# Kernel tuning notes

Hardware: AMD Instinct MI355X
Metric: run time of the kernel (lower is better)

## Reference

```python
import jax, jax.numpy as jnp
import numpy as np
from math import factorial

MUL = 64
LS = (0, 1, 2)            # node irrep l's, each with multiplicity MUL
SH_LS = (0, 1, 2)         # edge spherical-harmonics l's (lmax=2)
NODE_DIM = MUL * sum(2 * l + 1 for l in LS)  # 576
# uvu instructions (i_node, j_sh, k_out) from the original selection rule ir_k in ir_i*ir_j
INSTRUCTIONS = [(0, 0, 0), (0, 1, 1), (0, 2, 2), (1, 0, 1), (1, 1, 0), (1, 1, 2),
                (1, 2, 1), (2, 0, 2), (2, 1, 1), (2, 2, 0), (2, 2, 2)]
N_PATHS = {0: 3, 1: 4, 2: 4}          # number of instructions writing each output irrep
N_TP_W = len(INSTRUCTIONS) * MUL      # 704 per-edge TP weights
N_NODES, N_EDGES = 10000, 100000


def _su2_cg(j1, j2, j3, m1, m2, m3):
    # Clebsch-Gordan <j1 m1 j2 m2 | j3 m3> via Racah formula (integer j)
    if m1 + m2 != m3:
        return 0.0
    f = factorial
    pref = ((2 * j3 + 1)
            * f(j1 + j2 - j3) * f(j1 - j2 + j3) * f(-j1 + j2 + j3) / f(j1 + j2 + j3 + 1)
            * f(j1 + m1) * f(j1 - m1) * f(j2 + m2) * f(j2 - m2) * f(j3 + m3) * f(j3 - m3)) ** 0.5
    s = 0.0
    for k in range(0, j1 + j2 + j3 + 1):
        d = [k, j1 + j2 - j3 - k, j1 - m1 - k, j2 + m2 - k, j3 - j2 + m1 + k, j3 - j1 - m2 + k]
        if any(t < 0 for t in d):
            continue
        s += (-1) ** k / np.prod([float(f(t)) for t in d])
    return pref * s


def _q(l):
    # real -> complex spherical harmonic change of basis (e3nn convention, phase makes CG real)
    q = np.zeros((2 * l + 1, 2 * l + 1), dtype=complex)
    for m in range(-l, 0):
        q[l + m, l + abs(m)] = 1 / 2 ** 0.5
        q[l + m, l - abs(m)] = -1j / 2 ** 0.5
    q[l, l] = 1.0
    for m in range(1, l + 1):
        q[l + m, l + abs(m)] = (-1) ** m / 2 ** 0.5
        q[l + m, l - abs(m)] = 1j * (-1) ** m / 2 ** 0.5
    return (-1j) ** l * q


def _real_cg(l1, l2, l3):
    cg = np.zeros((2 * l1 + 1, 2 * l2 + 1, 2 * l3 + 1), dtype=complex)
    for a, m1 in enumerate(range(-l1, l1 + 1)):
        for b, m2 in enumerate(range(-l2, l2 + 1)):
            for c, m3 in enumerate(range(-l3, l3 + 1)):
                cg[a, b, c] = _su2_cg(l1, l2, l3, m1, m2, m3)
    C = np.einsum('ij,kl,nm,ikn->jlm', _q(l1), _q(l2), np.conj(_q(l3)), cg)
    C = C.real if np.abs(C.real).sum() >= np.abs(C.imag).sum() else C.imag
    return jnp.asarray(C / np.linalg.norm(C), dtype=jnp.float32)  # Frobenius-normalized (3j-style)


W3J = {}
for (_i, _j, _k) in INSTRUCTIONS:
    _key = (LS[_i], SH_LS[_j], LS[_k])
    if _key not in W3J:
        W3J[_key] = _real_cg(*_key)


def _sh(u):
    # component-normalized real spherical harmonics up to l=2 on unit vectors u: [E,3] -> [E,9]
    x, y, z = u[:, 0], u[:, 1], u[:, 2]
    s3 = 3.0 ** 0.5
    sh0 = jnp.ones_like(x)[:, None]
    sh1 = s3 * jnp.stack([y, z, x], -1)
    sh2 = 5.0 ** 0.5 * jnp.stack([s3 * x * y, s3 * y * z, 1.5 * z * z - 0.5,
                                  s3 * x * z, 0.5 * s3 * (x * x - y * y)], -1)
    return jnp.concatenate([sh0, sh1, sh2], -1)


def _blocks(t):
    # split [N, 576] into per-l blocks [N, MUL, 2l+1]
    out, off = [], 0
    for l in LS:
        d = 2 * l + 1
        out.append(t[:, off:off + MUL * d].reshape(-1, MUL, d))
        off += MUL * d
    return out


def _forward(node_feat, edge_vec, fc_w0, fc_w1, fc_w2, lin_w, src, dst):
    E, N = edge_vec.shape[0], node_feat.shape[0]
    dist = jnp.linalg.norm(edge_vec, axis=-1, keepdims=True)      # [E,1]
    sh = _sh(edge_vec / jnp.maximum(dist, 1e-9))                  # [E,9]
    # radial MLP (FullyConnectedNet-style: x @ W / sqrt(fan_in), silu on hidden layers)
    h = jax.nn.silu(dist @ fc_w0)
    h = jax.nn.silu(h @ fc_w1 / jnp.sqrt(64.0))
    tp_w = h @ fc_w2 / jnp.sqrt(64.0)                             # [E, 704]
    xb = _blocks(node_feat[src])                                  # gather source node feats
    sh_b, off = [], 0
    for l in SH_LS:
        d = 2 * l + 1
        sh_b.append(sh[:, off:off + d])
        off += d
    msg_b = [jnp.zeros((E, MUL, 2 * l + 1), node_feat.dtype) for l in LS]
    for n, (i, j, k) in enumerate(INSTRUCTIONS):                  # uvu channelwise tensor product
        C = W3J[(LS[i], SH_LS[j], LS[k])]
        w = tp_w[:, n * MUL:(n + 1) * MUL]                        # [E, MUL] per-edge path weights
        alpha = ((2 * LS[k] + 1.0) / N_PATHS[k]) ** 0.5           # component/path normalization
        msg_b[k] = msg_b[k] + alpha * jnp.einsum('abc,eua,eb,eu->euc', C, xb[i], sh_b[j], w)
    msg = jnp.concatenate([m.reshape(E, -1) for m in msg_b], -1)  # [E,576]
    aggr = jax.ops.segment_sum(msg, dst, num_segments=N)          # scatter-add over destination
    ab = _blocks(aggr)
    out = jnp.concatenate(
        [(jnp.einsum('nud,uv->nvd', ab[l], lin_w[l]) / MUL ** 0.5).reshape(N, -1)
         for l in range(len(LS))], -1)                            # equivariant Linear per irrep
    return out + node_feat                                        # residual


def setup_inputs() -> dict:
    key = jax.random.key(0)
    ks = jax.random.split(key, 8)
    return {
        'node_feat': jax.random.normal(ks[0], (N_NODES, NODE_DIM), jnp.float32),
        'edge_index': jax.random.randint(ks[1], (2, N_EDGES), 0, N_NODES),
        'edge_vec': jax.random.normal(ks[2], (N_EDGES, 3), jnp.float32),
        'fc_w0': jax.random.normal(ks[3], (1, 64), jnp.float32),
        'fc_w1': jax.random.normal(ks[4], (64, 64), jnp.float32),
        'fc_w2': jax.random.normal(ks[5], (64, N_TP_W), jnp.float32),
        'lin_w': jax.random.normal(ks[6], (len(LS), MUL, MUL), jnp.float32),
    }


def reference(node_feat, edge_index, edge_vec, fc_w0, fc_w1, fc_w2, lin_w):
    src, dst = edge_index[0], edge_index[1]
    return _forward(node_feat, edge_vec, fc_w0, fc_w1, fc_w2, lin_w, src, dst)
```

## Files before the change

kernel.cpp:

```cpp
#include <hip/hip_runtime.h>
#include <hip/hip_fp16.h>
#include <cmath>
#include <complex>

#define MULT 64
#define NODE_DIM 576
#define TE 8
#define PB 64

typedef _Float16 half8_t __attribute__((ext_vector_type(8)));
typedef _Float16 half4_t __attribute__((ext_vector_type(4)));
typedef float    floatx4 __attribute__((ext_vector_type(4)));

typedef std::complex<double> cd;

static double factd(int n){ double r=1; for(int i=2;i<=n;i++) r*=(double)i; return r; }

static double su2_cg(int j1,int j2,int j3,int m1,int m2,int m3){
  if(m1+m2!=m3) return 0.0;
  double pref = (2*j3+1)*factd(j1+j2-j3)*factd(j1-j2+j3)*factd(-j1+j2+j3)/factd(j1+j2+j3+1)
              * factd(j1+m1)*factd(j1-m1)*factd(j2+m2)*factd(j2-m2)*factd(j3+m3)*factd(j3-m3);
  pref = std::sqrt(pref);
  double s=0;
  for(int k=0;k<=j1+j2+j3;k++){
    int d0=k, d1=j1+j2-j3-k, d2=j1-m1-k, d3=j2+m2-k, d4=j3-j2+m1+k, d5=j3-j1-m2+k;
    if(d0<0||d1<0||d2<0||d3<0||d4<0||d5<0) continue;
    double denom = factd(d0)*factd(d1)*factd(d2)*factd(d3)*factd(d4)*factd(d5);
    s += ((k&1)?-1.0:1.0)/denom;
  }
  return pref*s;
}

static void make_q(int l, cd q[5][5]){
  for(int i=0;i<5;i++)for(int j=0;j<5;j++) q[i][j]=cd(0,0);
  double s = 1.0/std::sqrt(2.0);
  for(int m=-l;m<0;m++){
    q[l+m][l-m] = cd(s,0);
    q[l+m][l+m] = cd(0,-s);
  }
  q[l][l]=cd(1,0);
  for(int m=1;m<=l;m++){
    double sg = (m&1)?-1.0:1.0;
    q[l+m][l+m]=cd(sg*s,0);
    q[l+m][l-m]=cd(0,sg*s);
  }
  cd ph = (l==0)?cd(1,0) : ((l==1)?cd(0,-1) : cd(-1,0));
  for(int i=0;i<2*l+1;i++)for(int j=0;j<2*l+1;j++) q[i][j]*=ph;
}

static void real_cg(int l1,int l2,int l3, double* out){
  int d1=2*l1+1,d2=2*l2+1,d3=2*l3+1;
  double cg[125];
  for(int a=0;a<d1;a++)for(int b=0;b<d2;b++)for(int c=0;c<d3;c++)
    cg[(a*d2+b)*d3+c] = su2_cg(l1,l2,l3,a-l1,b-l2,c-l3);
  cd q1[5][5],q2[5][5],q3[5][5];
  make_q(l1,q1); make_q(l2,q2); make_q(l3,q3);
  cd C[125];
  for(int t=0;t<d1*d2*d3;t++) C[t]=cd(0,0);
  for(int i=0;i<d1;i++)for(int k=0;k<d2;k++)for(int n=0;n<d3;n++){
    double v = cg[(i*d2+k)*d3+n];
    if(v==0.0) continue;
    for(int j=0;j<d1;j++){
      cd a = q1[i][j]*v;
      if(a.real()==0.0 && a.imag()==0.0) continue;
      for(int l=0;l<d2;l++){
        cd b = a*q2[k][l];
        for(int m=0;m<d3;m++) C[(j*d2+l)*d3+m] += b*std::conj(q3[n][m]);
      }
    }
  }
  double sre=0,sim=0;
  for(int t=0;t<d1*d2*d3;t++){ sre+=std::fabs(C[t].real()); sim+=std::fabs(C[t].imag()); }
  bool use_re = (sre>=sim);
  double nrm=0;
  for(int t=0;t<d1*d2*d3;t++){ double x=use_re?C[t].real():C[t].imag(); nrm+=x*x; }
  nrm=std::sqrt(nrm);
  for(int t=0;t<d1*d2*d3;t++){ double x=use_re?C[t].real():C[t].imag(); out[t]=x/nrm; }
}

struct CGPack { float v[363]; };

__device__ __forceinline__ float silu_f(float x){ return x/(1.f+expf(-x)); }
__host__ __device__ constexpr int LOFF(int l){ return l==0?0:(l==1?1:4); }

template<int DI,int DJ,int DK>
__device__ __forceinline__ void tp_add(const float* __restrict__ C, const float* xi,
                                       const float* sh, float wn, float* mk){
  float tmp[DK];
#pragma unroll
  for(int c=0;c<DK;c++) tmp[c]=0.f;
#pragma unroll
  for(int a=0;a<DI;a++){
#pragma unroll
    for(int b=0;b<DJ;b++){
      float p = xi[a]*sh[b];
#pragma unroll
      for(int c=0;c<DK;c++) tmp[c] = fmaf(C[(a*DJ+b)*DK+c], p, tmp[c]);
    }
  }
#pragma unroll
  for(int c=0;c<DK;c++) mk[c] = fmaf(wn, tmp[c], mk[c]);
}

__global__ void hist_kernel(const int* __restrict__ dst, int* __restrict__ cnt, int E){
  int i = blockIdx.x*blockDim.x + threadIdx.x;
  if(i<E) atomicAdd(&cnt[dst[i]], 1);
}

__global__ __launch_bounds__(1024) void scan_kernel(const int* __restrict__ cnt,
                                                    int* __restrict__ row_ptr, int N){
  __shared__ int s_part[1024];
  const int t = threadIdx.x;
  const int per = (N + 1023) >> 10;
  const int b0 = t*per, b1 = min(N, b0+per);
  int local = 0;
  for(int i=b0;i<b1;i++) local += cnt[i];
  s_part[t] = local;
  __syncthreads();
  for(int off=1; off<1024; off<<=1){
    int v = (t>=off) ? s_part[t-off] : 0;
    __syncthreads();
    s_part[t] += v;
    __syncthreads();
  }
  int run = (t==0) ? 0 : s_part[t-1];
  for(int i=b0;i<b1;i++){ row_ptr[i] = run; run += cnt[i]; }
  if(t==1023) row_ptr[N] = s_part[1023];
}

__global__ void fill_kernel(const int* __restrict__ dst, const int* __restrict__ row_ptr,
                            int* __restrict__ cnt2, int* __restrict__ sorted, int E){
  int i = blockIdx.x*blockDim.x + threadIdx.x;
  if(i<E){
    int d = dst[i];
    int pos = atomicAdd(&cnt2[d], 1);
    sorted[row_ptr[d]+pos] = i;
  }
}

__global__ void sortb_kernel(int* __restrict__ sorted, const int* __restrict__ row_ptr, int N){
  int n = blockIdx.x*blockDim.x + threadIdx.x;
  if(n>=N) return;
  int b=row_ptr[n], e=row_ptr[n+1];
  for(int i=b+1;i<e;i++){
    int v=sorted[i]; int j=i-1;
    while(j>=b && sorted[j]>v){ sorted[j+1]=sorted[j]; j--; }
    sorted[j+1]=v;
  }
}

__global__ void w2t_kernel(const float* __restrict__ w2, __half* __restrict__ w2t){
  int i = blockIdx.x*256 + threadIdx.x;
  if(i < 704*64){
    int col = i >> 6, k = i & 63;
    w2t[i] = (__half)w2[k*704 + col];
  }
}

template<typename TW>
__global__ __launch_bounds__(256,2) void emp_pre4_kernel(
  const float* __restrict__ evec, const float* __restrict__ w0,
  const float* __restrict__ w1, const __half* __restrict__ w2t,
  TW* __restrict__ tpw, float* __restrict__ shs, int E)
{
  __shared__ float     s_h0T[64][64];
  __shared__ float     s_tile[64][64];
  __shared__ _Float16  s_h1h[64][64];
  __shared__ _Float16  s_w2t[64][64];
  __shared__ float     s_d[PB];

  const int t   = threadIdx.x;
  const int eg  = t >> 4;
  const int ug  = t & 15;
  const int es0 = eg*4, u0 = ug*4;
  const int e0  = blockIdx.x*PB;

  if(t < PB){
    const int e = e0 + t;
    float dist = 0.f;
    if(e < E){
      float ex=evec[e*3+0], ey=evec[e*3+1], ez=evec[e*3+2];
      dist = sqrtf(ex*ex+ey*ey+ez*ez);
      float inv = 1.f/fmaxf(dist,1e-9f);
      float x=ex*inv, y=ey*inv, z=ez*inv;
      const float s3=1.7320508075688772f, s5=2.2360679774997896f;
      float* srow = shs + (size_t)e*12;
      srow[0]=1.f;
      srow[1]=s3*y; srow[2]=s3*z; srow[3]=s3*x;
      srow[4]=s5*s3*x*y; srow[5]=s5*s3*y*z; srow[6]=s5*(1.5f*z*z-0.5f);
      srow[7]=s5*s3*x*z; srow[8]=s5*0.5f*s3*(x*x-y*y);
    }
    s_d[t] = dist;
  }
#pragma unroll
  for(int r=0;r<16;r++){ int idx=t+r*256; s_tile[idx>>6][idx&63] = w1[idx]; }
  __syncthreads();

#pragma unroll
  for(int r=0;r<16;r++){
    int idx = t + r*256;
    int u = idx>>6, es = idx&63;
    s_h0T[u][es] = silu_f(s_d[es]*w0[u]);
  }
  __syncthreads();

  {
    float acc[4][4];
#pragma unroll
    for(int i=0;i<4;i++)
#pragma unroll
      for(int j=0;j<4;j++) acc[i][j]=0.f;
#pragma unroll 4
    for(int k=0;k<64;k++){
      float4 a = *(const float4*)&s_h0T[k][es0];
      float4 b = *(const float4*)&s_tile[k][u0];
      float av[4]={a.x,a.y,a.z,a.w};
      float bv[4]={b.x,b.y,b.z,b.w};
#pragma unroll
      for(int i=0;i<4;i++)
#pragma unroll
        for(int j=0;j<4;j++) acc[i][j]=fmaf(av[i],bv[j],acc[i][j]);
    }
#pragma unroll
    for(int i=0;i<4;i++){
      const int row = es0+i;
      const int ks  = u0 ^ ((row&7)<<3);
      half4_t hv;
#pragma unroll
      for(int j=0;j<4;j++) hv[j] = (_Float16)silu_f(acc[i][j]*0.125f);
      *(half4_t*)&s_h1h[row][ks] = hv;
    }
  }
  __syncthreads();

  const int lane = t & 63;
  const int w    = t >> 6;
  const int lr   = lane & 15;
  const int lk   = lane >> 4;
  half8_t fA0, fA1;
  {
    const int row = w*16 + lr;
    const int swz = (row&7)<<3;
    fA0 = *(half8_t*)&s_h1h[row][(     lk*8) ^ swz];
    fA1 = *(half8_t*)&s_h1h[row][(32 + lk*8) ^ swz];
  }

  for(int n=0;n<11;n++){
    __syncthreads();
#pragma unroll
    for(int r=0;r<2;r++){
      int c8  = t + r*256;
      int col = c8 >> 3;
      int k8  = (c8 & 7) << 3;
      int ks  = k8 ^ ((col & 7) << 3);
      *(uint4*)&s_w2t[col][ks] =
        *(const uint4*)&w2t[(size_t)(n*64+col)*64 + k8];
    }
    __syncthreads();
#pragma unroll
    for(int cg=0; cg<4; cg++){
      const int colB = cg*16 + lr;
      const int swzB = (colB&7)<<3;
      half8_t fB0 = *(half8_t*)&s_w2t[colB][(     lk*8) ^ swzB];
      half8_t fB1 = *(half8_t*)&s_w2t[colB][(32 + lk*8) ^ swzB];
      floatx4 acc = {0.f,0.f,0.f,0.f};
      acc = __builtin_amdgcn_mfma_f32_16x16x32_f16(fA0, fB0, acc, 0,0,0);
      acc = __builtin_amdgcn_mfma_f32_16x16x32_f16(fA1, fB1, acc, 0,0,0);
#pragma unroll
      for(int r=0;r<4;r++){
        const int e = e0 + w*16 + lk*4 + r;
        if(e < E) tpw[(size_t)e*704 + n*64 + cg*16 + lr] = (TW)(acc[r]*0.125f);
      }
    }
  }
}

template<typename TW>
__global__ __launch_bounds__(256,1) void emp_gather4_kernel(
  const float* __restrict__ nf, const TW* __restrict__ tpw,
  const float* __restrict__ shs, const int* __restrict__ sorted,
  const int* __restrict__ row_ptr, const int* __restrict__ src_idx,
  const float* __restrict__ lw, float* __restrict__ out, int NN, CGPack cgp)
{
  __shared__ float s_a[4][NODE_DIM];
  const int t = threadIdx.x;
  const int u = t & 63;
  const int w = t >> 6;
  const int n = blockIdx.x*4 + w;
  const bool vn = (n < NN);

  float H0[1]={0.f}, H1[3]={0.f}, H2[5]={0.f}, H3[3]={0.f}, H4[9]={0.f},
        H5[9]={0.f}, H6[15]={0.f}, H7[5]={0.f}, H8[15]={0.f},
        H9[25]={0.f}, H10[25]={0.f};

#define ACC(N_, XA, DI, DJ, JO, WN, SH)                                      \
      {                                                                      \
        const float wnl = WN[N_];                                            \
        _Pragma("unroll")                                                    \
        for(int b=0;b<(DJ);b++){                                             \
          float z = wnl*SH[(JO)+b];                                          \
          _Pragma("unroll")                                                  \
          for(int a=0;a<(DI);a++)                                            \
            H##N_[a*(DJ)+b] = fmaf(XA[a], z, H##N_[a*(DJ)+b]);               \
        }                                                                    \
      }
#define ACC_ALL(X0, X1, X2, WN, SH)                                          \
      ACC(0, X0,1,1,0,WN,SH) ACC(1, X0,1,3,1,WN,SH) ACC(2, X0,1,5,4,WN,SH)   \
      ACC(3, X1,3,1,0,WN,SH) ACC(4, X1,3,3,1,WN,SH) ACC(5, X1,3,3,1,WN,SH)   \
      ACC(6, X1,3,5,4,WN,SH) ACC(7, X2,5,1,0,WN,SH) ACC(8, X2,5,3,1,WN,SH)   \
      ACC(9, X2,5,5,4,WN,SH) ACC(10,X2,5,5,4,WN,SH)

  if(vn){
    const int beg = row_ptr[n], end = row_ptr[n+1];
    int i = beg;
    for(; i+1<end; i+=2){
      const int eA = __builtin_amdgcn_readfirstlane(sorted[i]);
      const int eB = __builtin_amdgcn_readfirstlane(sorted[i+1]);
      const int sA = __builtin_amdgcn_readfirstlane(src_idx[eA]);
      const int sB = __builtin_amdgcn_readfirstlane(src_idx[eB]);
      const float* xrA = nf + (size_t)sA*NODE_DIM;
      const float* xrB = nf + (size_t)sB*NODE_DIM;
      const TW*    wrA = tpw + (size_t)eA*704;
      const TW*    wrB = tpw + (size_t)eB*704;
      const float* srA = shs + (size_t)eA*12;
      const float* srB = shs + (size_t)eB*12;
      float x0A[1]={xrA[u]}, x0B[1]={xrB[u]};
      float x1A[3], x1B[3], x2A[5], x2B[5], shA[9], shB[9], wnA[11], wnB[11];
#pragma unroll
      for(int a=0;a<3;a++){ x1A[a]=xrA[64+u*3+a]; x1B[a]=xrB[64+u*3+a]; }
#pragma unroll
      for(int a=0;a<5;a++){ x2A[a]=xrA[256+u*5+a]; x2B[a]=xrB[256+u*5+a]; }
#pragma unroll
      for(int j=0;j<9;j++){ shA[j]=srA[j]; shB[j]=srB[j]; }
#pragma unroll
      for(int m=0;m<11;m++){ wnA[m]=(float)wrA[m*64+u]; wnB[m]=(float)wrB[m*64+u]; }
      ACC_ALL(x0A,x1A,x2A,wnA,shA)
      ACC_ALL(x0B,x1B,x2B,wnB,shB)
    }
    if(i<end){
      const int eA = __builtin_amdgcn_readfirstlane(sorted[i]);
      const int sA = __builtin_amdgcn_readfirstlane(src_idx[eA]);
      const float* xrA = nf + (size_t)sA*NODE_DIM;
      const TW*    wrA = tpw + (size_t)eA*704;
      const float* srA = shs + (size_t)eA*12;
      float x0A[1]={xrA[u]};
      float x1A[3], x2A[5], shA[9], wnA[11];
#pragma unroll
      for(int a=0;a<3;a++) x1A[a]=xrA[64+u*3+a];
#pragma unroll
      for(int a=0;a<5;a++) x2A[a]=xrA[256+u*5+a];
#pragma unroll
      for(int j=0;j<9;j++) shA[j]=srA[j];
#pragma unroll
      for(int m=0;m<11;m++) wnA[m]=(float)wrA[m*64+u];
      ACC_ALL(x0A,x1A,x2A,wnA,shA)
    }
  }
#undef ACC_ALL
#undef ACC

  float mg[9];
#pragma unroll
  for(int i=0;i<9;i++) mg[i]=0.f;
#define CGA(N_, DI, DJ, DK, OFF, KO)                                         \
  _Pragma("unroll")                                                          \
  for(int a=0;a<(DI);a++)                                                    \
    _Pragma("unroll")                                                        \
    for(int b=0;b<(DJ);b++){                                                 \
      float h = H##N_[a*(DJ)+b];                                             \
      _Pragma("unroll")                                                      \
      for(int c=0;c<(DK);c++)                                                \
        mg[(KO)+c] = fmaf(cgp.v[(OFF)+(a*(DJ)+b)*(DK)+c], h, mg[(KO)+c]);    \
    }
  CGA(0, 1,1,1, 0,   0)
  CGA(1, 1,3,3, 1,   1)
  CGA(2, 1,5,5, 10,  4)
  CGA(3, 3,1,3, 35,  1)
  CGA(4, 3,3,1, 44,  0)
  CGA(5, 3,3,5, 53,  4)
  CGA(6, 3,5,3, 98,  1)
  CGA(7, 5,1,5, 143, 4)
  CGA(8, 5,3,3, 168, 1)
  CGA(9, 5,5,1, 213, 0)
  CGA(10,5,5,5, 238, 4)
#undef CGA

  s_a[w][u] = mg[0];
#pragma unroll
  for(int d=0;d<3;d++) s_a[w][(1+d)*64+u] = mg[1+d];
#pragma unroll
  for(int d=0;d<5;d++) s_a[w][(4+d)*64+u] = mg[4+d];
  __syncthreads();

  if(vn){
    const int v = u;
    float o0=0.f, o1[3]={0.f,0.f,0.f}, o2[5]={0.f,0.f,0.f,0.f,0.f};
#pragma unroll 8
    for(int uu=0;uu<64;uu++){
      float wv0 = lw[uu*64+v];
      o0 = fmaf(s_a[w][uu], wv0, o0);
      float wv1 = lw[4096+uu*64+v];
#pragma unroll
      for(int d=0;d<3;d++) o1[d]=fmaf(s_a[w][(1+d)*64+uu],wv1,o1[d]);
      float wv2 = lw[8192+uu*64+v];
#pragma unroll
      for(int d=0;d<5;d++) o2[d]=fmaf(s_a[w][(4+d)*64+uu],wv2,o2[d]);
    }
    const float* nrow = nf + (size_t)n*NODE_DIM;
    float* orow = out + (size_t)n*NODE_DIM;
    orow[v] = fmaf(o0,0.125f,nrow[v]);
#pragma unroll
    for(int d=0;d<3;d++) orow[64+v*3+d]=fmaf(o1[d],0.125f,nrow[64+v*3+d]);
#pragma unroll
    for(int d=0;d<5;d++) orow[256+v*5+d]=fmaf(o2[d],0.125f,nrow[256+v*5+d]);
  }
}

__global__ __launch_bounds__(64) void emp_node_kernel(
  const float* __restrict__ nf, const float* __restrict__ lw,
  float* __restrict__ out, int N)
{
  __shared__ float s_a[NODE_DIM];
  const int n = blockIdx.x;
  const int v = threadIdx.x;
  float* orow = out + (size_t)n*NODE_DIM;
#pragma unroll
  for(int r=0;r<9;r++) s_a[r*64+v] = orow[r*64+v];
  __syncthreads();

  float o0=0.f, o1[3]={0.f,0.f,0.f}, o2[5]={0.f,0.f,0.f,0.f,0.f};
#pragma unroll 8
  for(int uu=0;uu<64;uu++){
    float wv0 = lw[uu*64+v];
    o0 = fmaf(s_a[uu], wv0, o0);
    float wv1 = lw[4096+uu*64+v];
#pragma unroll
    for(int d=0;d<3;d++) o1[d]=fmaf(s_a[64+uu*3+d],wv1,o1[d]);
    float wv2 = lw[8192+uu*64+v];
#pragma unroll
    for(int d=0;d<5;d++) o2[d]=fmaf(s_a[256+uu*5+d],wv2,o2[d]);
  }
  const float* nrow = nf + (size_t)n*NODE_DIM;
  orow[v] = fmaf(o0,0.125f,nrow[v]);
#pragma unroll
  for(int d=0;d<3;d++) orow[64+v*3+d]=fmaf(o1[d],0.125f,nrow[64+v*3+d]);
#pragma unroll
  for(int d=0;d<5;d++) orow[256+v*5+d]=fmaf(o2[d],0.125f,nrow[256+v*5+d]);
}

__global__ __launch_bounds__(512,1) void emp_pre_kernel(
  const float* __restrict__ evec, const float* __restrict__ w0,
  const float* __restrict__ w1, float* __restrict__ h1s,
  float* __restrict__ shs, int E)
{
  __shared__ float s_h0[TE][64];
  __shared__ float s_sh[TE][9];
  const int t=threadIdx.x, u=t&63, es=t>>6;
  const int e = blockIdx.x*TE+es;
  const bool valid = (e<E);
  float dist=0.f;
  if(valid){
    float ex=evec[e*3+0], ey=evec[e*3+1], ez=evec[e*3+2];
    dist = sqrtf(ex*ex+ey*ey+ez*ez);
    if(u==0){
      float inv = 1.f/fmaxf(dist,1e-9f);
      float x=ex*inv, y=ey*inv, z=ez*inv;
      const float s3=1.7320508075688772f, s5=2.2360679774997896f;
      s_sh[es][0]=1.f;
      s_sh[es][1]=s3*y; s_sh[es][2]=s3*z; s_sh[es][3]=s3*x;
      s_sh[es][4]=s5*s3*x*y; s_sh[es][5]=s5*s3*y*z; s_sh[es][6]=s5*(1.5f*z*z-0.5f);
      s_sh[es][7]=s5*s3*x*z; s_sh[es][8]=s5*0.5f*s3*(x*x-y*y);
    }
  }
  s_h0[es][u] = silu_f(dist * w0[u]);
  __syncthreads();
  if(valid && u<9) shs[(size_t)e*12+u] = s_sh[es][u];
  float acc = 0.f;
#pragma unroll
  for(int k=0;k<64;k++) acc = fmaf(s_h0[es][k], w1[k*64+u], acc);
  if(valid) h1s[(size_t)e*64+u] = silu_f(acc*0.125f);
}

__global__ __launch_bounds__(256,2) void emp_gather_kernel(
  const float* __restrict__ nf, const float* __restrict__ h1s,
  const float* __restrict__ shs, const int* __restrict__ sorted,
  const int* __restrict__ row_ptr, const int* __restrict__ src_idx,
  const float* __restrict__ w2, float* __restrict__ aggr, CGPack cgp)
{
  __shared__ float s_tile[64][64];
  __shared__ float s_x[8][576];
  __shared__ float s_h1[8][64];
  __shared__ float s_sh[8][12];
  __shared__ int   s_eid[8];
  __shared__ int   s_src[8];
  __shared__ float s_red[4][576];

  const int n = blockIdx.x;
  const int t = threadIdx.x;
  const int u = t & 63;
  const int w = t >> 6;
  const int beg = row_ptr[n], end = row_ptr[n+1];

  float mg[9];
#pragma unroll
  for(int i=0;i<9;i++) mg[i]=0.f;

  for(int base=beg; base<end; base+=8){
    const int C = min(8, end-base);
    if(t < C){ int e = sorted[base+t]; s_eid[t]=e; s_src[t]=src_idx[e]; }
    __syncthreads();
    for(int idx=t; idx<C*576; idx+=256){
      int c = idx/576, j = idx - 576*c;
      s_x[c][j] = nf[(size_t)s_src[c]*NODE_DIM + j];
    }
    for(int idx=t; idx<C*64; idx+=256){
      int c = idx>>6, j = idx&63;
      s_h1[c][j] = h1s[(size_t)s_eid[c]*64 + j];
    }
    if(t < C*12){
      int c = t/12, j = t - 12*c;
      if(j<9) s_sh[c][j] = shs[(size_t)s_eid[c]*12 + j];
    }
    __syncthreads();

#define GI(N_, LI, LJ, LK, OFF)                                              \
    {                                                                        \
      for(int idx=t; idx<4096; idx+=256){                                    \
        int k = idx>>6, j = idx&63;                                          \
        s_tile[k][j] = w2[k*704 + (N_)*64 + j];                              \
      }                                                                      \
      __syncthreads();                                                       \
      for(int c=w; c<C; c+=4){                                               \
        float wn = 0.f;                                                      \
        _Pragma("unroll")                                                    \
        for(int k=0;k<64;k++) wn = fmaf(s_h1[c][k], s_tile[k][u], wn);       \
        wn *= 0.125f;                                                        \
        const int xb = (LI)==0 ? u : ((LI)==1 ? 64+u*3 : 256+u*5);           \
        tp_add<2*(LI)+1,2*(LJ)+1,2*(LK)+1>(cgp.v+(OFF), &s_x[c][xb],         \
                                           &s_sh[c][LOFF(LJ)], wn,           \
                                           mg+LOFF(LK));                     \
      }                                                                      \
      __syncthreads();                                                       \
    }
    GI(0,0,0,0,0)
    GI(1,0,1,1,1)
    GI(2,0,2,2,10)
    GI(3,1,0,1,35)
    GI(4,1,1,0,44)
    GI(5,1,1,2,53)
    GI(6,1,2,1,98)
    GI(7,2,0,2,143)
    GI(8,2,1,1,168)
    GI(9,2,2,0,213)
    GI(10,2,2,2,238)
#undef GI
  }

  s_red[w][u] = mg[0];
#pragma unroll
  for(int a=0;a<3;a++) s_red[w][64+u*3+a] = mg[1+a];
#pragma unroll
  for(int a=0;a<5;a++) s_red[w][256+u*5+a] = mg[4+a];
  __syncthreads();
  float* arow = aggr + (size_t)n*NODE_DIM;
  for(int idx=t; idx<NODE_DIM; idx+=256)
    arow[idx] = s_red[0][idx]+s_red[1][idx]+s_red[2][idx]+s_red[3][idx];
}

extern "C" void kernel_launch(void* const* d_in, const int* in_sizes, int n_in,
                              void* d_out, int out_size, void* d_ws, size_t ws_size,
                              hipStream_t stream)
{
  const float* nf   = (const float*)d_in[0];
  const int*   eidx = (const int*)  d_in[1];
  const float* evec = (const float*)d_in[2];
  const float* w0   = (const float*)d_in[3];
  const float* w1   = (const float*)d_in[4];
  const float* w2   = (const float*)d_in[5];
  const float* lw   = (const float*)d_in[6];
  const int E = in_sizes[1]/2;
  const int N = in_sizes[0]/NODE_DIM;
  const int* src = eidx;
  const int* dst = eidx + E;

  CGPack cgp;
  {
    const int II[11]={0,0,0,1,1,1,1,2,2,2,2};
    const int JJ[11]={0,1,2,0,1,1,2,0,1,2,2};
    const int KK[11]={0,1,2,1,0,2,1,2,1,0,2};
    const int OFF[11]={0,1,10,35,44,53,98,143,168,213,238};
    const double npaths[3]={3.0,4.0,4.0};
    double tmp[125];
    for(int n=0;n<11;n++){
      int li=II[n], lj=JJ[n], lk=KK[n];
      real_cg(li,lj,lk,tmp);
      double alpha = std::sqrt((2.0*lk+1.0)/npaths[lk]);
      int sz=(2*li+1)*(2*lj+1)*(2*lk+1);
      for(int q=0;q<sz;q++) cgp.v[OFF[n]+q]=(float)(tmp[q]*alpha);
    }
  }

  auto align256 = [](size_t x){ return (x + 255) & ~(size_t)255; };

  auto layoutA = [&](size_t elemBytes, size_t& o_tpw, size_t& o_sh, size_t& o_w2t,
                     size_t& o_srt, size_t& o_cnt, size_t& o_rp)->size_t{
    size_t off = 0;
    o_tpw = off; off = align256(off + (size_t)E*704*elemBytes);
    o_sh  = off; off = align256(off + (size_t)E*12*sizeof(float));
    o_w2t = off; off = align256(off + (size_t)704*64*sizeof(__half));
    o_srt = off; off = align256(off + (size_t)E*sizeof(int));
    o_cnt = off; off = align256(off + (size_t)N*2*sizeof(int));
    o_rp  = off; off = align256(off + (size_t)(N+1)*sizeof(int));
    return off;
  };
  size_t a32_tpw,a32_sh,a32_w2t,a32_srt,a32_cnt,a32_rp;
  size_t a16_tpw,a16_sh,a16_w2t,a16_srt,a16_cnt,a16_rp;
  const size_t needA32 = layoutA(4, a32_tpw,a32_sh,a32_w2t,a32_srt,a32_cnt,a32_rp);
  const size_t needA16 = layoutA(2, a16_tpw,a16_sh,a16_w2t,a16_srt,a16_cnt,a16_rp);

  size_t offB = 0;
  size_t b_h1  = offB; offB = align256(offB + (size_t)E*64*sizeof(float));
  size_t b_sh  = offB; offB = align256(offB + (size_t)E*12*sizeof(float));
  size_t b_srt = offB; offB = align256(offB + (size_t)E*sizeof(int));
  size_t b_cnt = offB; offB = align256(offB + (size_t)N*2*sizeof(int));
  size_t b_rp  = offB; offB = align256(offB + (size_t)(N+1)*sizeof(int));

  char* ws = (char*)d_ws;

  auto runCSR = [&](int* cnt, int* cnt2, int* row_ptr, int* sorted){
    hipMemsetAsync(cnt, 0, (size_t)N*2*sizeof(int), stream);
    hipLaunchKernelGGL(hist_kernel, dim3((E+255)/256), dim3(256), 0, stream,
                       dst, cnt, E);
    hipLaunchKernelGGL(scan_kernel, dim3(1), dim3(1024), 0, stream,
                       cnt, row_ptr, N);
    hipLaunchKernelGGL(fill_kernel, dim3((E+255)/256), dim3(256), 0, stream,
                       dst, row_ptr, cnt2, sorted, E);
    hipLaunchKernelGGL(sortb_kernel, dim3((N+255)/256), dim3(256), 0, stream,
                       sorted, row_ptr, N);
  };

  const int nb3 = (N+3)/4;

  if(ws_size >= needA32){
    float*  tpw    = (float*) (ws + a32_tpw);
    float*  shs    = (float*) (ws + a32_sh);
    __half* w2t    = (__half*)(ws + a32_w2t);
    int*    sorted = (int*)   (ws + a32_srt);
    int*    cnt    = (int*)   (ws + a32_cnt);
    int*    cnt2   = cnt + N;
    int*    row_ptr= (int*)   (ws + a32_rp);
    hipLaunchKernelGGL(w2t_kernel, dim3((704*64+255)/256), dim3(256), 0, stream, w2, w2t);
    runCSR(cnt, cnt2, row_ptr, sorted);
    hipLaunchKernelGGL((emp_pre4_kernel<float>), dim3((E+PB-1)/PB), dim3(256), 0, stream,
                       evec, w0, w1, w2t, tpw, shs, E);
    hipLaunchKernelGGL((emp_gather4_kernel<float>), dim3(nb3), dim3(256), 0, stream,
                       nf, tpw, shs, sorted, row_ptr, src, lw, (float*)d_out, N, cgp);
  } else if(ws_size >= needA16){
    __half* tpw    = (__half*)(ws + a16_tpw);
    float*  shs    = (float*) (ws + a16_sh);
    __half* w2t    = (__half*)(ws + a16_w2t);
    int*    sorted = (int*)   (ws + a16_srt);
    int*    cnt    = (int*)   (ws + a16_cnt);
    int*    cnt2   = cnt + N;
    int*    row_ptr= (int*)   (ws + a16_rp);
    hipLaunchKernelGGL(w2t_kernel, dim3((704*64+255)/256), dim3(256), 0, stream, w2, w2t);
    runCSR(cnt, cnt2, row_ptr, sorted);
    hipLaunchKernelGGL((emp_pre4_kernel<__half>), dim3((E+PB-1)/PB), dim3(256), 0, stream,
                       evec, w0, w1, w2t, tpw, shs, E);
    hipLaunchKernelGGL((emp_gather4_kernel<__half>), dim3(nb3), dim3(256), 0, stream,
                       nf, tpw, shs, sorted, row_ptr, src, lw, (float*)d_out, N, cgp);
  } else {
    float* h1s    = (float*)(ws + b_h1);
    float* shs    = (float*)(ws + b_sh);
    int*   sorted = (int*)  (ws + b_srt);
    int*   cnt    = (int*)  (ws + b_cnt);
    int*   cnt2   = cnt + N;
    int*   row_ptr= (int*)  (ws + b_rp);
    runCSR(cnt, cnt2, row_ptr, sorted);
    hipLaunchKernelGGL(emp_pre_kernel, dim3((E+TE-1)/TE), dim3(512), 0, stream,
                       evec, w0, w1, h1s, shs, E);
    hipLaunchKernelGGL(emp_gather_kernel, dim3(N), dim3(256), 0, stream,
                       nf, h1s, shs, sorted, row_ptr, src, w2, (float*)d_out, cgp);
    hipLaunchKernelGGL(emp_node_kernel, dim3(N), dim3(64), 0, stream,
                       nf, lw, (float*)d_out, N);
  }
}
```

Baseline: 218.2 us.

## Store per-edge TP weights and SH in destination-sorted order, unroll gather by four

Adds a rank kernel that maps each edge to its position in the destination-sorted order and precomputes the sorted source indices. The pre kernel then writes per-edge TP weights and spherical harmonics at the sorted position, so the gather kernel reads them contiguously and skips the indirection through the sorted and src arrays. The gather loop is unrolled to four edges per iteration with vectorized SH loads to expose more memory-level parallelism. In exchange, the pre kernel's stores become scattered, an extra kernel launch is added, and register pressure rises in the gather.

```diff
diff --git a/kernel.cpp b/kernel.cpp
--- a/kernel.cpp
+++ b/kernel.cpp
@@ -149,6 +149,12 @@
   }
 }
 
+__global__ void rank_kernel(const int* __restrict__ sorted, const int* __restrict__ src_idx,
+                            int* __restrict__ rank, int* __restrict__ src_s, int E){
+  int i = blockIdx.x*blockDim.x + threadIdx.x;
+  if(i<E){ int e = sorted[i]; rank[e] = i; src_s[i] = src_idx[e]; }
+}
+
 __global__ void w2t_kernel(const float* __restrict__ w2, __half* __restrict__ w2t){
   int i = blockIdx.x*256 + threadIdx.x;
   if(i < 704*64){
@@ -161,6 +167,7 @@
 __global__ __launch_bounds__(256,2) void emp_pre4_kernel(
   const float* __restrict__ evec, const float* __restrict__ w0,
   const float* __restrict__ w1, const __half* __restrict__ w2t,
+  const int* __restrict__ rank,
   TW* __restrict__ tpw, float* __restrict__ shs, int E)
 {
   __shared__ float     s_h0T[64][64];
@@ -168,6 +175,7 @@
   __shared__ _Float16  s_h1h[64][64];
   __shared__ _Float16  s_w2t[64][64];
   __shared__ float     s_d[PB];
+  __shared__ int       s_rank[PB];
 
   const int t   = threadIdx.x;
   const int eg  = t >> 4;
@@ -178,19 +186,23 @@
   if(t < PB){
     const int e = e0 + t;
     float dist = 0.f;
+    int rk = 0;
     if(e < E){
+      rk = rank[e];
       float ex=evec[e*3+0], ey=evec[e*3+1], ez=evec[e*3+2];
       dist = sqrtf(ex*ex+ey*ey+ez*ez);
       float inv = 1.f/fmaxf(dist,1e-9f);
       float x=ex*inv, y=ey*inv, z=ez*inv;
       const float s3=1.7320508075688772f, s5=2.2360679774997896f;
-      float* srow = shs + (size_t)e*12;
+      float* srow = shs + (size_t)rk*12;
       srow[0]=1.f;
       srow[1]=s3*y; srow[2]=s3*z; srow[3]=s3*x;
       srow[4]=s5*s3*x*y; srow[5]=s5*s3*y*z; srow[6]=s5*(1.5f*z*z-0.5f);
       srow[7]=s5*s3*x*z; srow[8]=s5*0.5f*s3*(x*x-y*y);
+      srow[9]=0.f; srow[10]=0.f; srow[11]=0.f;
     }
     s_d[t] = dist;
+    s_rank[t] = rk;
   }
 #pragma unroll
   for(int r=0;r<16;r++){ int idx=t+r*256; s_tile[idx>>6][idx&63] = w1[idx]; }
@@ -268,19 +280,20 @@
       acc = __builtin_amdgcn_mfma_f32_16x16x32_f16(fA1, fB1, acc, 0,0,0);
 #pragma unroll
       for(int r=0;r<4;r++){
-        const int e = e0 + w*16 + lk*4 + r;
-        if(e < E) tpw[(size_t)e*704 + n*64 + cg*16 + lr] = (TW)(acc[r]*0.125f);
+        const int el = w*16 + lk*4 + r;
+        const int e  = e0 + el;
+        if(e < E) tpw[(size_t)s_rank[el]*704 + n*64 + cg*16 + lr] = (TW)(acc[r]*0.125f);
       }
     }
   }
 }
 
 template<typename TW>
-__global__ __launch_bounds__(256,1) void emp_gather4_kernel(
+__global__ __launch_bounds__(256,1) void emp_gather5_kernel(
   const float* __restrict__ nf, const TW* __restrict__ tpw,
-  const float* __restrict__ shs, const int* __restrict__ sorted,
-  const int* __restrict__ row_ptr, const int* __restrict__ src_idx,
-  const float* __restrict__ lw, float* __restrict__ out, int NN, CGPack cgp)
+  const float* __restrict__ shs, const int* __restrict__ src_s,
+  const int* __restrict__ row_ptr, const float* __restrict__ lw,
+  float* __restrict__ out, int NN, CGPack cgp)
 {
   __shared__ float s_a[4][NODE_DIM];
   const int t = threadIdx.x;
@@ -310,52 +323,51 @@
       ACC(6, X1,3,5,4,WN,SH) ACC(7, X2,5,1,0,WN,SH) ACC(8, X2,5,3,1,WN,SH)   \
       ACC(9, X2,5,5,4,WN,SH) ACC(10,X2,5,5,4,WN,SH)
 
+#define LOADE(S, I)                                                          \
+      const int s##S = __builtin_amdgcn_readfirstlane(src_s[I]);             \
+      const float* xr##S = nf + (size_t)s##S*NODE_DIM;                       \
+      const TW*    wr##S = tpw + (size_t)(I)*704;                            \
+      const float* sr##S = shs + (size_t)(I)*12;                             \
+      float x0##S[1]={xr##S[u]};                                             \
+      float x1##S[3], x2##S[5], sh##S[9], wn##S[11];                         \
+      _Pragma("unroll")                                                      \
+      for(int a=0;a<3;a++) x1##S[a]=xr##S[64+u*3+a];                         \
+      _Pragma("unroll")                                                      \
+      for(int a=0;a<5;a++) x2##S[a]=xr##S[256+u*5+a];                        \
+      { float4 p0=*(const float4*)&sr##S[0];                                 \
+        float4 p1=*(const float4*)&sr##S[4];                                 \
+        float  p2=sr##S[8];                                                  \
+        sh##S[0]=p0.x; sh##S[1]=p0.y; sh##S[2]=p0.z; sh##S[3]=p0.w;          \
+        sh##S[4]=p1.x; sh##S[5]=p1.y; sh##S[6]=p1.z; sh##S[7]=p1.w;          \
+        sh##S[8]=p2; }                                                       \
+      _Pragma("unroll")                                                      \
+      for(int m=0;m<11;m++) wn##S[m]=(float)wr##S[m*64+u];
+
   if(vn){
     const int beg = row_ptr[n], end = row_ptr[n+1];
     int i = beg;
-    for(; i+1<end; i+=2){
-      const int eA = __builtin_amdgcn_readfirstlane(sorted[i]);
-      const int eB = __builtin_amdgcn_readfirstlane(sorted[i+1]);
-      const int sA = __builtin_amdgcn_readfirstlane(src_idx[eA]);
-      const int sB = __builtin_amdgcn_readfirstlane(src_idx[eB]);
-      const float* xrA = nf + (size_t)sA*NODE_DIM;
-      const float* xrB = nf + (size_t)sB*NODE_DIM;
-      const TW*    wrA = tpw + (size_t)eA*704;
-      const TW*    wrB = tpw + (size_t)eB*704;
-      const float* srA = shs + (size_t)eA*12;
-      const float* srB = shs + (size_t)eB*12;
-      float x0A[1]={xrA[u]}, x0B[1]={xrB[u]};
-      float x1A[3], x1B[3], x2A[5], x2B[5], shA[9], shB[9], wnA[11], wnB[11];
-#pragma unroll
-      for(int a=0;a<3;a++){ x1A[a]=xrA[64+u*3+a]; x1B[a]=xrB[64+u*3+a]; }
-#pragma unroll
-      for(int a=0;a<5;a++){ x2A[a]=xrA[256+u*5+a]; x2B[a]=xrB[256+u*5+a]; }
-#pragma unroll
-      for(int j=0;j<9;j++){ shA[j]=srA[j]; shB[j]=srB[j]; }
-#pragma unroll
-      for(int m=0;m<11;m++){ wnA[m]=(float)wrA[m*64+u]; wnB[m]=(float)wrB[m*64+u]; }
+    for(; i+3<end; i+=4){
+      LOADE(A, i)
+      LOADE(B, i+1)
+      LOADE(C, i+2)
+      LOADE(D, i+3)
       ACC_ALL(x0A,x1A,x2A,wnA,shA)
       ACC_ALL(x0B,x1B,x2B,wnB,shB)
+      ACC_ALL(x0C,x1C,x2C,wnC,shC)
+      ACC_ALL(x0D,x1D,x2D,wnD,shD)
+    }
+    for(; i+1<end; i+=2){
+      LOADE(A, i)
+      LOADE(B, i+1)
+      ACC_ALL(x0A,x1A,x2A,wnA,shA)
+      ACC_ALL(x0B,x1B,x2B,wnB,shB)
     }
     if(i<end){
-      const int eA = __builtin_amdgcn_readfirstlane(sorted[i]);
-      const int sA = __builtin_amdgcn_readfirstlane(src_idx[eA]);
-      const float* xrA = nf + (size_t)sA*NODE_DIM;
-      const TW*    wrA = tpw + (size_t)eA*704;
-      const float* srA = shs + (size_t)eA*12;
-      float x0A[1]={xrA[u]};
-      float x1A[3], x2A[5], shA[9], wnA[11];
-#pragma unroll
-      for(int a=0;a<3;a++) x1A[a]=xrA[64+u*3+a];
-#pragma unroll
-      for(int a=0;a<5;a++) x2A[a]=xrA[256+u*5+a];
-#pragma unroll
-      for(int j=0;j<9;j++) shA[j]=srA[j];
-#pragma unroll
-      for(int m=0;m<11;m++) wnA[m]=(float)wrA[m*64+u];
+      LOADE(A, i)
       ACC_ALL(x0A,x1A,x2A,wnA,shA)
     }
   }
+#undef LOADE
 #undef ACC_ALL
 #undef ACC
 
@@ -603,20 +615,23 @@
   auto align256 = [](size_t x){ return (x + 255) & ~(size_t)255; };
 
   auto layoutA = [&](size_t elemBytes, size_t& o_tpw, size_t& o_sh, size_t& o_w2t,
-                     size_t& o_srt, size_t& o_cnt, size_t& o_rp)->size_t{
+                     size_t& o_srt, size_t& o_rnk, size_t& o_srs,
+                     size_t& o_cnt, size_t& o_rp)->size_t{
     size_t off = 0;
     o_tpw = off; off = align256(off + (size_t)E*704*elemBytes);
     o_sh  = off; off = align256(off + (size_t)E*12*sizeof(float));
     o_w2t = off; off = align256(off + (size_t)704*64*sizeof(__half));
     o_srt = off; off = align256(off + (size_t)E*sizeof(int));
+    o_rnk = off; off = align256(off + (size_t)E*sizeof(int));
+    o_srs = off; off = align256(off + (size_t)E*sizeof(int));
     o_cnt = off; off = align256(off + (size_t)N*2*sizeof(int));
     o_rp  = off; off = align256(off + (size_t)(N+1)*sizeof(int));
     return off;
   };
-  size_t a32_tpw,a32_sh,a32_w2t,a32_srt,a32_cnt,a32_rp;
-  size_t a16_tpw,a16_sh,a16_w2t,a16_srt,a16_cnt,a16_rp;
-  const size_t needA32 = layoutA(4, a32_tpw,a32_sh,a32_w2t,a32_srt,a32_cnt,a32_rp);
-  const size_t needA16 = layoutA(2, a16_tpw,a16_sh,a16_w2t,a16_srt,a16_cnt,a16_rp);
+  size_t a32_tpw,a32_sh,a32_w2t,a32_srt,a32_rnk,a32_srs,a32_cnt,a32_rp;
+  size_t a16_tpw,a16_sh,a16_w2t,a16_srt,a16_rnk,a16_srs,a16_cnt,a16_rp;
+  const size_t needA32 = layoutA(4, a32_tpw,a32_sh,a32_w2t,a32_srt,a32_rnk,a32_srs,a32_cnt,a32_rp);
+  const size_t needA16 = layoutA(2, a16_tpw,a16_sh,a16_w2t,a16_srt,a16_rnk,a16_srs,a16_cnt,a16_rp);
 
   size_t offB = 0;
   size_t b_h1  = offB; offB = align256(offB + (size_t)E*64*sizeof(float));
@@ -646,29 +661,37 @@
     float*  shs    = (float*) (ws + a32_sh);
     __half* w2t    = (__half*)(ws + a32_w2t);
     int*    sorted = (int*)   (ws + a32_srt);
+    int*    rank   = (int*)   (ws + a32_rnk);
+    int*    src_s  = (int*)   (ws + a32_srs);
     int*    cnt    = (int*)   (ws + a32_cnt);
     int*    cnt2   = cnt + N;
     int*    row_ptr= (int*)   (ws + a32_rp);
     hipLaunchKernelGGL(w2t_kernel, dim3((704*64+255)/256), dim3(256), 0, stream, w2, w2t);
     runCSR(cnt, cnt2, row_ptr, sorted);
+    hipLaunchKernelGGL(rank_kernel, dim3((E+255)/256), dim3(256), 0, stream,
+                       sorted, src, rank, src_s, E);
     hipLaunchKernelGGL((emp_pre4_kernel<float>), dim3((E+PB-1)/PB), dim3(256), 0, stream,
-                       evec, w0, w1, w2t, tpw, shs, E);
-    hipLaunchKernelGGL((emp_gather4_kernel<float>), dim3(nb3), dim3(256), 0, stream,
-                       nf, tpw, shs, sorted, row_ptr, src, lw, (float*)d_out, N, cgp);
+                       evec, w0, w1, w2t, rank, tpw, shs, E);
+    hipLaunchKernelGGL((emp_gather5_kernel<float>), dim3(nb3), dim3(256), 0, stream,
+                       nf, tpw, shs, src_s, row_ptr, lw, (float*)d_out, N, cgp);
   } else if(ws_size >= needA16){
     __half* tpw    = (__half*)(ws + a16_tpw);
     float*  shs    = (float*) (ws + a16_sh);
     __half* w2t    = (__half*)(ws + a16_w2t);
     int*    sorted = (int*)   (ws + a16_srt);
+    int*    rank   = (int*)   (ws + a16_rnk);
+    int*    src_s  = (int*)   (ws + a16_srs);
     int*    cnt    = (int*)   (ws + a16_cnt);
     int*    cnt2   = cnt + N;
     int*    row_ptr= (int*)   (ws + a16_rp);
     hipLaunchKernelGGL(w2t_kernel, dim3((704*64+255)/256), dim3(256), 0, stream, w2, w2t);
     runCSR(cnt, cnt2, row_ptr, sorted);
+    hipLaunchKernelGGL(rank_kernel, dim3((E+255)/256), dim3(256), 0, stream,
+                       sorted, src, rank, src_s, E);
     hipLaunchKernelGGL((emp_pre4_kernel<__half>), dim3((E+PB-1)/PB), dim3(256), 0, stream,
-                       evec, w0, w1, w2t, tpw, shs, E);
-    hipLaunchKernelGGL((emp_gather4_kernel<__half>), dim3(nb3), dim3(256), 0, stream,
-                       nf, tpw, shs, sorted, row_ptr, src, lw, (float*)d_out, N, cgp);
+                       evec, w0, w1, w2t, rank, tpw, shs, E);
+    hipLaunchKernelGGL((emp_gather5_kernel<__half>), dim3(nb3), dim3(256), 0, stream,
+                       nf, tpw, shs, src_s, row_ptr, lw, (float*)d_out, N, cgp);
   } else {
     float* h1s    = (float*)(ws + b_h1);
     float* shs    = (float*)(ws + b_sh);
```

Measured after the change: 321.3 us. 47.3% more time.
